# Kernel optimization log

Hardware: AMD Instinct MI355X
Metric: run time of the kernel (lower is better)

## Reference

```python
import jax, jax.numpy as jnp
import numpy as np


def setup_inputs() -> dict:
    key = jax.random.key(0)
    k1, k2 = jax.random.split(key)
    n_points = 32768
    n_elements = 2048
    # evaluation points in [0, 1)
    x_eval = jax.random.uniform(k1, (n_points, 1), dtype=jnp.float32)
    # sorted node coordinates (monotone 1D mesh on [0, 1))
    x_full = jnp.sort(jax.random.uniform(k2, (n_elements + 1,), dtype=jnp.float32))
    return {"x_eval": x_eval, "x_full": x_full}


def reference(x_eval, x_full):
    # Vectorized over all elements at once (original loops in Python per element).
    # xa = x_full[i], xb = x_full[i+1] for each of the E = n_nodes-1 elements.
    xa = x_full[:-1]                      # [E]
    xb = x_full[1:]                       # [E]
    h = xb - xa                           # [E]
    # layer1 = relu(-x + xb); layer2 = relu(-layer1/(h+eps) + 1)
    layer1 = jax.nn.relu(xb[None, :] - x_eval)            # [P, E] (x_eval is [P,1])
    layer2 = jax.nn.relu(1.0 - layer1 / (h[None, :] + 1e-9))  # [P, E]
    N0_tilde = 1.0 - layer2               # [P, E]  (w3=-1, b3=1)
    N1_tilde = layer2                     # [P, E]  (w3=+1, b3=0)
    first = N0_tilde[:, 0:1]              # [P, 1]
    last = N1_tilde[:, -1:]               # [P, 1]
    n_nodes = x_full.shape[0]
    if n_nodes > 2:
        internal = N0_tilde[:, 1:] + N1_tilde[:, :-1] - 1.0  # [P, E-1]
        return jnp.concatenate([first, internal, last], axis=1)  # [P, n_nodes]
    return jnp.concatenate([first, last], axis=1)
```

## Files before the change

### kernel.cpp

```cpp
#include <hip/hip_runtime.h>


__global__ void scatter_hats(const float* __restrict__ x_eval,
                             const float* __restrict__ x_full,
                             float* __restrict__ out,
                             int n_points, int n_nodes) {
    extern __shared__ float s_xf[];
    for (int i = threadIdx.x; i < n_nodes; i += blockDim.x) s_xf[i] = x_full[i];
    __syncthreads();

    int p = blockIdx.x * blockDim.x + threadIdx.x;
    if (p >= n_points) return;

    float x = x_eval[p];

    int lo = 0, hi = n_nodes;
    while (lo < hi) {
        int mid = (lo + hi) >> 1;
        if (s_xf[mid] <= x) lo = mid + 1; else hi = mid;
    }
    int e0 = lo - 1;
    if (e0 < 0) e0 = 0;
    int emax = n_nodes - 2;
    if (e0 > emax) e0 = emax;

    float xa = s_xf[e0];
    float xb = s_xf[e0 + 1];
    float l1   = fmaxf(xb - x, 0.0f);
    float frac = fmaxf(1.0f - l1 / (xb - xa + 1e-9f), 0.0f);

    size_t base = (size_t)p * (size_t)n_nodes;
    out[base + e0]     = 1.0f - frac;
    out[base + e0 + 1] = frac;
}

extern "C" void kernel_launch(void* const* d_in, const int* in_sizes, int n_in,
                              void* d_out, int out_size, void* d_ws, size_t ws_size,
                              hipStream_t stream) {
    const float* x_eval = (const float*)d_in[0];
    const float* x_full = (const float*)d_in[1];
    float* out = (float*)d_out;

    int n_points = in_sizes[0];
    int n_nodes  = in_sizes[1];

    hipMemsetAsync(d_out, 0, (size_t)out_size * sizeof(float), stream);

    int block = 256;
    int grid  = (n_points + block - 1) / block;
    size_t smem = (size_t)n_nodes * sizeof(float);
    scatter_hats<<<grid, block, smem, stream>>>(x_eval, x_full, out, n_points, n_nodes);
}
```

Measured before the change: 257.6 us.

## Fuse zero-fill and hat scatter into one vectorized row-writing kernel

Replaces the memset plus scatter kernel with a kernel that handles four rows per block. It computes each row's two nonzero hat values up front, then writes the full rows with float4 stores that select zero or the hat value. This removes the separate memset pass and the uncoalesced scatter writes. In exchange, each block first runs a serial binary search in global memory before streaming its output.

```diff
diff --git a/kernel.cpp b/kernel.cpp
--- a/kernel.cpp
+++ b/kernel.cpp
@@ -1,5 +1,65 @@
 #include <hip/hip_runtime.h>
 
+
+__global__ __launch_bounds__(256) void fused_rows4(
+        const float* __restrict__ x_eval,
+        const float* __restrict__ x_full,
+        float* __restrict__ out,
+        int n_points, int n_nodes) {
+    __shared__ int   s_e0[4];
+    __shared__ float s_a[4], s_b[4];
+
+    const int p0 = blockIdx.x * 4;
+
+    if (threadIdx.x < 4) {
+        int p = p0 + threadIdx.x;
+        float x = x_eval[p];
+        int lo = 0, hi = n_nodes;
+        while (lo < hi) {
+            int mid = (lo + hi) >> 1;
+            if (x_full[mid] <= x) lo = mid + 1; else hi = mid;
+        }
+        int e0 = lo - 1;
+        if (e0 < 0) e0 = 0;
+        int emax = n_nodes - 2;
+        if (e0 > emax) e0 = emax;
+        float xa = x_full[e0];
+        float xb = x_full[e0 + 1];
+        float l1   = fmaxf(xb - x, 0.0f);
+        float frac = fmaxf(1.0f - l1 / (xb - xa + 1e-9f), 0.0f);
+        s_e0[threadIdx.x] = e0;
+        s_a[threadIdx.x]  = 1.0f - frac;
+        s_b[threadIdx.x]  = frac;
+    }
+    __syncthreads();
+
+    const int   e00 = s_e0[0], e01 = s_e0[1], e02 = s_e0[2], e03 = s_e0[3];
+    const float a0 = s_a[0], a1 = s_a[1], a2 = s_a[2], a3 = s_a[3];
+    const float b0 = s_b[0], b1 = s_b[1], b2 = s_b[2], b3 = s_b[3];
+    const int n1 = n_nodes, n2 = 2 * n_nodes, n3 = 3 * n_nodes;
+    const int t0 = e00, t1 = n1 + e01, t2 = n2 + e02, t3 = n3 + e03;
+
+    float4* obase = (float4*)(out + (size_t)p0 * (size_t)n_nodes);
+    for (int q = threadIdx.x; q < n_nodes; q += 256) {
+        const int f0 = q << 2;
+        float v[4];
+#pragma unroll
+        for (int k = 0; k < 4; ++k) {
+            const int f = f0 + k;
+            float v0 = 0.0f;
+            v0 = (f == t0)     ? a0 : v0;
+            v0 = (f == t0 + 1) ? b0 : v0;
+            v0 = (f == t1)     ? a1 : v0;
+            v0 = (f == t1 + 1) ? b1 : v0;
+            v0 = (f == t2)     ? a2 : v0;
+            v0 = (f == t2 + 1) ? b2 : v0;
+            v0 = (f == t3)     ? a3 : v0;
+            v0 = (f == t3 + 1) ? b3 : v0;
+            v[k] = v0;
+        }
+        obase[q] = make_float4(v[0], v[1], v[2], v[3]);
+    }
+}
 
 __global__ void scatter_hats(const float* __restrict__ x_eval,
                              const float* __restrict__ x_full,
@@ -8,12 +68,9 @@
     extern __shared__ float s_xf[];
     for (int i = threadIdx.x; i < n_nodes; i += blockDim.x) s_xf[i] = x_full[i];
     __syncthreads();
-
     int p = blockIdx.x * blockDim.x + threadIdx.x;
     if (p >= n_points) return;
-
     float x = x_eval[p];
-
     int lo = 0, hi = n_nodes;
     while (lo < hi) {
         int mid = (lo + hi) >> 1;
@@ -23,12 +80,10 @@
     if (e0 < 0) e0 = 0;
     int emax = n_nodes - 2;
     if (e0 > emax) e0 = emax;
-
     float xa = s_xf[e0];
     float xb = s_xf[e0 + 1];
     float l1   = fmaxf(xb - x, 0.0f);
     float frac = fmaxf(1.0f - l1 / (xb - xa + 1e-9f), 0.0f);
-
     size_t base = (size_t)p * (size_t)n_nodes;
     out[base + e0]     = 1.0f - frac;
     out[base + e0 + 1] = frac;
@@ -44,10 +99,14 @@
     int n_points = in_sizes[0];
     int n_nodes  = in_sizes[1];
 
-    hipMemsetAsync(d_out, 0, (size_t)out_size * sizeof(float), stream);
-
-    int block = 256;
-    int grid  = (n_points + block - 1) / block;
-    size_t smem = (size_t)n_nodes * sizeof(float);
-    scatter_hats<<<grid, block, smem, stream>>>(x_eval, x_full, out, n_points, n_nodes);
+    if ((n_points % 4) == 0 && n_nodes >= 2) {
+        int grid = n_points / 4;
+        fused_rows4<<<grid, 256, 0, stream>>>(x_eval, x_full, out, n_points, n_nodes);
+    } else {
+        hipMemsetAsync(d_out, 0, (size_t)out_size * sizeof(float), stream);
+        int block = 256;
+        int grid  = (n_points + block - 1) / block;
+        size_t smem = (size_t)n_nodes * sizeof(float);
+        scatter_hats<<<grid, block, smem, stream>>>(x_eval, x_full, out, n_points, n_nodes);
+    }
 }
```

After: 262.0 us. Within noise of the previous version (+1.7%).
